# Kernel optimization log

Measured on AMD Instinct MI355X. Metric: run time of the kernel, lower is better.

Reference implementation:

```python
import jax, jax.numpy as jnp
import numpy as np

N_NODES = 20000
N_EDGES = 640000
C_IN = 128      # num_node_features
K_FOLDS = 8     # num_edge_features
FILTERS = 128


def setup_inputs() -> dict:
    key = jax.random.key(0)
    k1, k2, k3, k4, k5, k6 = jax.random.split(key, 6)
    node_features = jax.random.normal(k1, (N_NODES, C_IN), dtype=jnp.float32)
    edge_features = jax.random.uniform(k2, (K_FOLDS, N_EDGES), dtype=jnp.float32)
    rows = jax.random.randint(k3, (N_EDGES,), 0, N_NODES)
    cols = jax.random.randint(k4, (N_EDGES,), 0, N_NODES)
    indices = jnp.stack([rows, cols], axis=1).astype(jnp.int64)
    # glorot_uniform kernel [K, C_in, filters]
    limit = np.sqrt(6.0 / (C_IN + FILTERS))
    kernel = jax.random.uniform(k5, (K_FOLDS, C_IN, FILTERS), dtype=jnp.float32,
                                minval=-limit, maxval=limit)
    bias = jnp.zeros((FILTERS,), dtype=jnp.float32)
    return {
        "node_features": node_features,
        "edge_features": edge_features,
        "kernel": kernel,
        "bias": bias,
        "indices": indices,
        "out_size": N_NODES,
    }


def reference(node_features, edge_features, kernel, bias, indices, out_size):
    # fold_conv: out[i,f] = sum_{e: row(e)=i} sum_k ef[k,e] * (x[col(e)] @ kernel[k])[f]
    row = indices[:, 0]
    col = indices[:, 1]
    xg = node_features[col]  # [E, C] gathered source-node features
    E = xg.shape[0]
    msgs = jnp.zeros((E, kernel.shape[2]), dtype=node_features.dtype)
    # Loop over the small fixed number of folds (K=8); each iteration is a
    # dense [E,C]x[C,F] matmul scaled by the per-edge fold weight.
    for k in range(kernel.shape[0]):
        msgs = msgs + (xg @ kernel[k]) * edge_features[k][:, None]
    out = jax.ops.segment_sum(msgs, row, num_segments=out_size)  # [out_size, F]
    out = out + bias  # bias_add; activation is None (linear)
    return out
```

## Files before the change

### kernel.cpp

```cpp
#include <hip/hip_runtime.h>
#include <cstddef>
#include <cstdint>

static constexpr int kNodes   = 20000;
static constexpr int kEdges   = 640000;
static constexpr int kCin     = 128;
static constexpr int kFolds   = 8;
static constexpr int kFilters = 128;
static constexpr int kKdim    = kFolds * kCin;
static constexpr int kCap     = 80;

static constexpr int kNBucketF = 1250;
static constexpr int kCapF     = 768;
static constexpr int kBin1Blk  = 160;

typedef __attribute__((ext_vector_type(8))) short v8s;
typedef __attribute__((ext_vector_type(4))) float v4f;

__device__ __forceinline__ unsigned short f2bf(float f) {
    union { float f; uint32_t u; } v; v.f = f;
    const uint32_t u = v.u;
    return (unsigned short)((u + 0x7fffu + ((u >> 16) & 1u)) >> 16);
}
__device__ __forceinline__ float bf2f(unsigned short s) {
    union { uint32_t u; float f; } v; v.u = ((uint32_t)s) << 16;
    return v.f;
}

__global__ __launch_bounds__(256) void prep_k(
    const int2*  __restrict__ idx2,
    const float* __restrict__ ef,
    const float* __restrict__ x,
    const float* __restrict__ W,
    int* __restrict__ bucketCnt,
    unsigned int* __restrict__ pairs,
    unsigned int* __restrict__ rec,
    unsigned short* __restrict__ xb,
    unsigned short* __restrict__ Wp)
{
    const int b = blockIdx.x;
    const int t = threadIdx.x;
    if (b < kBin1Blk) {
        __shared__ int hist[kNBucketF];
        __shared__ int base[kNBucketF];
        const int e0 = b * 4096;

        for (int i = t; i < kNBucketF; i += 256) hist[i] = 0;
        __syncthreads();

        int rows[16];
        #pragma unroll
        for (int i = 0; i < 16; ++i) {
            const int e = e0 + i * 256 + t;
            int row = -1;
            if (e < kEdges) {
                row = idx2[e].x;
                atomicAdd(&hist[row >> 4], 1);
            }
            rows[i] = row;
        }
        __syncthreads();

        for (int i = t; i < kNBucketF; i += 256) {
            const int h = hist[i];
            base[i] = h ? atomicAdd(&bucketCnt[i], h) : 0;
            hist[i] = 0;
        }
        __syncthreads();

        #pragma unroll
        for (int i = 0; i < 16; ++i) {
            const int row = rows[i];
            if (row >= 0) {
                const int e  = e0 + i * 256 + t;
                const int bk = row >> 4;
                const int sl = base[bk] + atomicAdd(&hist[bk], 1);
                if (sl < kCapF)
                    pairs[(size_t)bk * kCapF + sl] =
                        ((unsigned)(row & 15) << 24) | (unsigned)e;
            }
        }
    } else if (b < 2660) {
        const int e = (b - kBin1Blk) * 256 + t;
        const int2 rc = idx2[e];
        union { uint4 q; unsigned int w[4]; unsigned short s[8]; } o;
        #pragma unroll
        for (int k = 0; k < kFolds; ++k)
            o.s[k] = f2bf(ef[(size_t)k * kEdges + e]);
        uint4* recp = (uint4*)(rec + (size_t)e * 8);
        recp[0] = make_uint4((unsigned)rc.y, o.w[0], o.w[1], o.w[2]);
        recp[1] = make_uint4(o.w[3], 0u, 0u, 0u);
    } else if (b < 3910) {
        const int i = (b - 2660) * 2048 + t * 8;
        const float4 a = *(const float4*)(x + i);
        const float4 c = *(const float4*)(x + i + 4);
        union { uint4 q; unsigned short s[8]; } o;
        o.s[0] = f2bf(a.x); o.s[1] = f2bf(a.y); o.s[2] = f2bf(a.z); o.s[3] = f2bf(a.w);
        o.s[4] = f2bf(c.x); o.s[5] = f2bf(c.y); o.s[6] = f2bf(c.z); o.s[7] = f2bf(c.w);
        *(uint4*)(xb + i) = o.q;
    } else {
        const int t2 = (b - 3910) * 256 + t;
        const int n  = t2 & 127;
        const int k8 = t2 >> 7;
        const int c  = k8 >> 2;
        const int q  = k8 & 3;
        union { uint4 qv; unsigned short s[8]; } o;
        #pragma unroll
        for (int j = 0; j < 8; ++j)
            o.s[j] = f2bf(W[(size_t)(k8 * 8 + j) * kFilters + n]);
        *(uint4*)(Wp + (((size_t)c * kFilters + n) * 4 + q) * 8) = o.qv;
    }
}

static constexpr int kSWS2 = 1048;

__global__ __launch_bounds__(256) void pull_k(
    const unsigned short* __restrict__ xb,
    const unsigned int* __restrict__ pairs,
    const int*  __restrict__ bucketCnt,
    const unsigned int* __restrict__ rec,
    const unsigned short* __restrict__ Wp,
    const float* __restrict__ bias,
    float* __restrict__ out)
{
    __shared__ int sCol[16][kCap + 4];
    __shared__ int sDeg[16];
    __shared__ int sCnt[16];
    __shared__ __align__(16) char arena[16 * (kCap + 4) * 8 * 4];

    float (*sEf)[kCap + 4][8] = (float(*)[kCap + 4][8])arena;
    unsigned short (*sS)[kSWS2] = (unsigned short(*)[kSWS2])arena;

    const int t  = threadIdx.x;
    const int B  = blockIdx.x;
    const int n0 = B * 16;

    if (t < 16) sCnt[t] = 0;
    __syncthreads();
    {
        int nseg = bucketCnt[B];
        nseg = nseg < kCapF ? nseg : kCapF;
        const unsigned int* seg = pairs + (size_t)B * kCapF;
        for (int s = t; s < nseg; s += 256) {
            const unsigned p = seg[s];
            const int rl = (int)(p >> 24);
            const int c  = atomicAdd(&sCnt[rl], 1);
            if (c < kCap) sCol[rl][c] = (int)(p & 0xFFFFFFu);
        }
    }
    __syncthreads();

    {
        const int g16 = t >> 4;
        const int s0  = t & 15;
        int dg = sCnt[g16];
        dg = dg < kCap ? dg : kCap;
        for (int s = s0; s < dg; s += 16) {
            const int e = sCol[g16][s];
            const uint4 q0    = *(const uint4*)(rec + (size_t)e * 8);
            const unsigned w3 = rec[(size_t)e * 8 + 4];
            sCol[g16][s] = (int)q0.x;
            sEf[g16][s][0] = bf2f((unsigned short)(q0.y));
            sEf[g16][s][1] = bf2f((unsigned short)(q0.y >> 16));
            sEf[g16][s][2] = bf2f((unsigned short)(q0.z));
            sEf[g16][s][3] = bf2f((unsigned short)(q0.z >> 16));
            sEf[g16][s][4] = bf2f((unsigned short)(q0.w));
            sEf[g16][s][5] = bf2f((unsigned short)(q0.w >> 16));
            sEf[g16][s][6] = bf2f((unsigned short)(w3));
            sEf[g16][s][7] = bf2f((unsigned short)(w3 >> 16));
        }
        const int dgP = (dg + 3) & ~3;
        for (int s = dg + s0; s < dgP; s += 16) {
            sCol[g16][s] = 0;
            #pragma unroll
            for (int k = 0; k < kFolds; ++k) sEf[g16][s][k] = 0.f;
        }
        if (s0 == 0) sDeg[g16] = dg;
    }
    __syncthreads();

    const int wave = t >> 6;
    const int lane = t & 63;
    const int g    = lane >> 4;
    const int c8   = (lane & 15) * 8;
    const int ln   = wave * 4 + g;
    const int degP = (sDeg[ln] + 3) & ~3;

    float acc[8][8];
    #pragma unroll
    for (int k = 0; k < 8; ++k)
        #pragma unroll
        for (int j = 0; j < 8; ++j) acc[k][j] = 0.f;

    const unsigned short* xbase = xb + c8;

    auto proc = [&](v8s xv, int i) {
        float xf[8];
        #pragma unroll
        for (int jj = 0; jj < 8; ++jj) xf[jj] = bf2f((unsigned short)xv[jj]);
        const float4 wa = *(const float4*)&sEf[ln][i][0];
        const float4 wc = *(const float4*)&sEf[ln][i][4];
        const float w[8] = {wa.x, wa.y, wa.z, wa.w, wc.x, wc.y, wc.z, wc.w};
        #pragma unroll
        for (int k = 0; k < 8; ++k)
            #pragma unroll
            for (int jj = 0; jj < 8; ++jj)
                acc[k][jj] += w[k] * xf[jj];
    };

    v8s x0 = (v8s)0, x1 = (v8s)0, x2 = (v8s)0, x3 = (v8s)0;
    if (degP > 0) {
        x0 = *(const v8s*)(xbase + (size_t)sCol[ln][0] * kCin);
        x1 = *(const v8s*)(xbase + (size_t)sCol[ln][1] * kCin);
        x2 = *(const v8s*)(xbase + (size_t)sCol[ln][2] * kCin);
        x3 = *(const v8s*)(xbase + (size_t)sCol[ln][3] * kCin);
    }

    for (int i = 0; i < degP; i += 4) {
        const int j = (i + 4 < degP) ? (i + 4) : i;
        const v8s y0 = *(const v8s*)(xbase + (size_t)sCol[ln][j]     * kCin);
        const v8s y1 = *(const v8s*)(xbase + (size_t)sCol[ln][j + 1] * kCin);
        const v8s y2 = *(const v8s*)(xbase + (size_t)sCol[ln][j + 2] * kCin);
        const v8s y3 = *(const v8s*)(xbase + (size_t)sCol[ln][j + 3] * kCin);

        proc(x0, i); proc(x1, i + 1); proc(x2, i + 2); proc(x3, i + 3);

        x0 = y0; x1 = y1; x2 = y2; x3 = y3;
    }

    __syncthreads();
    #pragma unroll
    for (int k = 0; k < 8; ++k) {
        union { uint4 q; unsigned short s[8]; } o;
        #pragma unroll
        for (int j = 0; j < 8; ++j) o.s[j] = f2bf(acc[k][j]);
        *(uint4*)&sS[ln][k * kCin + c8] = o.q;
    }
    __syncthreads();

    const int quad = lane >> 4;
    const int r16  = lane & 15;

    v4f acc2[2];
    acc2[0] = (v4f){0.f, 0.f, 0.f, 0.f};
    acc2[1] = (v4f){0.f, 0.f, 0.f, 0.f};

    const unsigned short* wb0 = Wp + (((size_t)(wave * 32 + r16)) * 4 + quad) * 8;
    const unsigned short* wb1 = wb0 + 16 * 4 * 8;

    #pragma unroll 4
    for (int c = 0; c < 32; ++c) {
        const v8s a  = *(const v8s*)&sS[r16][c * 32 + quad * 8];
        const v8s b0 = *(const v8s*)(wb0 + (size_t)c * kFilters * 32);
        const v8s b1 = *(const v8s*)(wb1 + (size_t)c * kFilters * 32);
        acc2[0] = __builtin_amdgcn_mfma_f32_16x16x32_bf16(a, b0, acc2[0], 0, 0, 0);
        acc2[1] = __builtin_amdgcn_mfma_f32_16x16x32_bf16(a, b1, acc2[1], 0, 0, 0);
    }

    #pragma unroll
    for (int i = 0; i < 2; ++i) {
        const int n  = (wave * 2 + i) * 16 + r16;
        const float bv = bias[n];
        #pragma unroll
        for (int r = 0; r < 4; ++r) {
            const int m = n0 + quad * 4 + r;
            out[(size_t)m * kFilters + n] = acc2[i][r] + bv;
        }
    }
}

extern "C" void kernel_launch(void* const* d_in, const int* in_sizes, int n_in,
                              void* d_out, int out_size, void* d_ws, size_t ws_size,
                              hipStream_t stream) {
    const float* x    = (const float*)d_in[0];
    const float* ef   = (const float*)d_in[1];
    const float* W    = (const float*)d_in[2];
    const float* bias = (const float*)d_in[3];
    const int2*  idx2 = (const int2*)d_in[4];
    float* out = (float*)d_out;

    char* ws = (char*)d_ws;
    unsigned int*   pairs  = (unsigned int*)(ws);
    int*            bucketCnt = (int*)(ws + 3840000);
    unsigned int*   rec    = (unsigned int*)(ws + 40960000);
    unsigned short* xb     = (unsigned short*)(ws + 67840000);
    unsigned short* Wp     = (unsigned short*)(ws + 72960000);

    hipMemsetAsync(bucketCnt, 0, kNBucketF * sizeof(int), stream);

    prep_k<<<3974, 256, 0, stream>>>(idx2, ef, x, W, bucketCnt,
                                     pairs, rec, xb, Wp);
    pull_k<<<kNodes / 16, 256, 0, stream>>>(xb, pairs, bucketCnt, rec,
                                            Wp, bias, out);
}
```

Baseline: 153.6 us.

## Halve nodes per pull block to double grid size and cut register use

Row buckets now hold 8 destination nodes instead of 16, so the pull kernel launches 2500 blocks instead of 1250. Each wave gathers 2 nodes, with 32 lanes per node each handling 4 channels, which halves the accumulator registers per thread. The aim is better occupancy and more even load across compute units. In exchange, half of the MFMA rows are zero-padded and wasted, gathers use narrower 8-byte loads, and the packed weight matrix is read from L2 by twice as many blocks.

```diff
diff --git a/kernel.cpp b/kernel.cpp
--- a/kernel.cpp
+++ b/kernel.cpp
@@ -10,11 +10,12 @@
 static constexpr int kKdim    = kFolds * kCin;
 static constexpr int kCap     = 80;
 
-static constexpr int kNBucketF = 1250;
-static constexpr int kCapF     = 768;
+static constexpr int kNBucketF = 2500;
+static constexpr int kCapF     = 384;
 static constexpr int kBin1Blk  = 160;
 
 typedef __attribute__((ext_vector_type(8))) short v8s;
+typedef __attribute__((ext_vector_type(4))) short v4s;
 typedef __attribute__((ext_vector_type(4))) float v4f;
 
 __device__ __forceinline__ unsigned short f2bf(float f) {
@@ -55,7 +56,7 @@
             int row = -1;
             if (e < kEdges) {
                 row = idx2[e].x;
-                atomicAdd(&hist[row >> 4], 1);
+                atomicAdd(&hist[row >> 3], 1);
             }
             rows[i] = row;
         }
@@ -73,11 +74,11 @@
             const int row = rows[i];
             if (row >= 0) {
                 const int e  = e0 + i * 256 + t;
-                const int bk = row >> 4;
+                const int bk = row >> 3;
                 const int sl = base[bk] + atomicAdd(&hist[bk], 1);
                 if (sl < kCapF)
                     pairs[(size_t)bk * kCapF + sl] =
-                        ((unsigned)(row & 15) << 24) | (unsigned)e;
+                        ((unsigned)(row & 7) << 24) | (unsigned)e;
             }
         }
     } else if (b < 2660) {
@@ -123,19 +124,19 @@
     const float* __restrict__ bias,
     float* __restrict__ out)
 {
-    __shared__ int sCol[16][kCap + 4];
-    __shared__ int sDeg[16];
-    __shared__ int sCnt[16];
-    __shared__ __align__(16) char arena[16 * (kCap + 4) * 8 * 4];
+    __shared__ int sCol[8][kCap + 4];
+    __shared__ int sDeg[8];
+    __shared__ int sCnt[8];
+    __shared__ __align__(16) char arena[8 * (kCap + 4) * 8 * 4];
 
     float (*sEf)[kCap + 4][8] = (float(*)[kCap + 4][8])arena;
     unsigned short (*sS)[kSWS2] = (unsigned short(*)[kSWS2])arena;
 
     const int t  = threadIdx.x;
     const int B  = blockIdx.x;
-    const int n0 = B * 16;
-
-    if (t < 16) sCnt[t] = 0;
+    const int n0 = B * 8;
+
+    if (t < 8) sCnt[t] = 0;
     __syncthreads();
     {
         int nseg = bucketCnt[B];
@@ -151,77 +152,78 @@
     __syncthreads();
 
     {
-        const int g16 = t >> 4;
-        const int s0  = t & 15;
-        int dg = sCnt[g16];
+        const int g8 = t >> 5;
+        const int s0 = t & 31;
+        int dg = sCnt[g8];
         dg = dg < kCap ? dg : kCap;
-        for (int s = s0; s < dg; s += 16) {
-            const int e = sCol[g16][s];
+        for (int s = s0; s < dg; s += 32) {
+            const int e = sCol[g8][s];
             const uint4 q0    = *(const uint4*)(rec + (size_t)e * 8);
             const unsigned w3 = rec[(size_t)e * 8 + 4];
-            sCol[g16][s] = (int)q0.x;
-            sEf[g16][s][0] = bf2f((unsigned short)(q0.y));
-            sEf[g16][s][1] = bf2f((unsigned short)(q0.y >> 16));
-            sEf[g16][s][2] = bf2f((unsigned short)(q0.z));
-            sEf[g16][s][3] = bf2f((unsigned short)(q0.z >> 16));
-            sEf[g16][s][4] = bf2f((unsigned short)(q0.w));
-            sEf[g16][s][5] = bf2f((unsigned short)(q0.w >> 16));
-            sEf[g16][s][6] = bf2f((unsigned short)(w3));
-            sEf[g16][s][7] = bf2f((unsigned short)(w3 >> 16));
+            sCol[g8][s] = (int)q0.x;
+            sEf[g8][s][0] = bf2f((unsigned short)(q0.y));
+            sEf[g8][s][1] = bf2f((unsigned short)(q0.y >> 16));
+            sEf[g8][s][2] = bf2f((unsigned short)(q0.z));
+            sEf[g8][s][3] = bf2f((unsigned short)(q0.z >> 16));
+            sEf[g8][s][4] = bf2f((unsigned short)(q0.w));
+            sEf[g8][s][5] = bf2f((unsigned short)(q0.w >> 16));
+            sEf[g8][s][6] = bf2f((unsigned short)(w3));
+            sEf[g8][s][7] = bf2f((unsigned short)(w3 >> 16));
         }
         const int dgP = (dg + 3) & ~3;
-        for (int s = dg + s0; s < dgP; s += 16) {
-            sCol[g16][s] = 0;
+        for (int s = dg + s0; s < dgP; s += 32) {
+            sCol[g8][s] = 0;
             #pragma unroll
-            for (int k = 0; k < kFolds; ++k) sEf[g16][s][k] = 0.f;
-        }
-        if (s0 == 0) sDeg[g16] = dg;
+            for (int k = 0; k < kFolds; ++k) sEf[g8][s][k] = 0.f;
+        }
+        if (s0 == 0) sDeg[g8] = dg;
     }
     __syncthreads();
 
     const int wave = t >> 6;
     const int lane = t & 63;
-    const int g    = lane >> 4;
-    const int c8   = (lane & 15) * 8;
-    const int ln   = wave * 4 + g;
+    const int g2   = lane >> 5;
+    const int chl  = lane & 31;
+    const int c4   = chl * 4;
+    const int ln   = wave * 2 + g2;
     const int degP = (sDeg[ln] + 3) & ~3;
 
-    float acc[8][8];
+    float acc[8][4];
     #pragma unroll
     for (int k = 0; k < 8; ++k)
         #pragma unroll
-        for (int j = 0; j < 8; ++j) acc[k][j] = 0.f;
-
-    const unsigned short* xbase = xb + c8;
-
-    auto proc = [&](v8s xv, int i) {
-        float xf[8];
-        #pragma unroll
-        for (int jj = 0; jj < 8; ++jj) xf[jj] = bf2f((unsigned short)xv[jj]);
+        for (int j = 0; j < 4; ++j) acc[k][j] = 0.f;
+
+    const unsigned short* xbase = xb + c4;
+
+    auto proc = [&](v4s xv, int i) {
+        float xf[4];
+        #pragma unroll
+        for (int jj = 0; jj < 4; ++jj) xf[jj] = bf2f((unsigned short)xv[jj]);
         const float4 wa = *(const float4*)&sEf[ln][i][0];
         const float4 wc = *(const float4*)&sEf[ln][i][4];
         const float w[8] = {wa.x, wa.y, wa.z, wa.w, wc.x, wc.y, wc.z, wc.w};
         #pragma unroll
         for (int k = 0; k < 8; ++k)
             #pragma unroll
-            for (int jj = 0; jj < 8; ++jj)
+            for (int jj = 0; jj < 4; ++jj)
                 acc[k][jj] += w[k] * xf[jj];
     };
 
-    v8s x0 = (v8s)0, x1 = (v8s)0, x2 = (v8s)0, x3 = (v8s)0;
+    v4s x0 = (v4s)0, x1 = (v4s)0, x2 = (v4s)0, x3 = (v4s)0;
     if (degP > 0) {
-        x0 = *(const v8s*)(xbase + (size_t)sCol[ln][0] * kCin);
-        x1 = *(const v8s*)(xbase + (size_t)sCol[ln][1] * kCin);
-        x2 = *(const v8s*)(xbase + (size_t)sCol[ln][2] * kCin);
-        x3 = *(const v8s*)(xbase + (size_t)sCol[ln][3] * kCin);
+        x0 = *(const v4s*)(xbase + (size_t)sCol[ln][0] * kCin);
+        x1 = *(const v4s*)(xbase + (size_t)sCol[ln][1] * kCin);
+        x2 = *(const v4s*)(xbase + (size_t)sCol[ln][2] * kCin);
+        x3 = *(const v4s*)(xbase + (size_t)sCol[ln][3] * kCin);
     }
 
     for (int i = 0; i < degP; i += 4) {
         const int j = (i + 4 < degP) ? (i + 4) : i;
-        const v8s y0 = *(const v8s*)(xbase + (size_t)sCol[ln][j]     * kCin);
-        const v8s y1 = *(const v8s*)(xbase + (size_t)sCol[ln][j + 1] * kCin);
-        const v8s y2 = *(const v8s*)(xbase + (size_t)sCol[ln][j + 2] * kCin);
-        const v8s y3 = *(const v8s*)(xbase + (size_t)sCol[ln][j + 3] * kCin);
+        const v4s y0 = *(const v4s*)(xbase + (size_t)sCol[ln][j]     * kCin);
+        const v4s y1 = *(const v4s*)(xbase + (size_t)sCol[ln][j + 1] * kCin);
+        const v4s y2 = *(const v4s*)(xbase + (size_t)sCol[ln][j + 2] * kCin);
+        const v4s y3 = *(const v4s*)(xbase + (size_t)sCol[ln][j + 3] * kCin);
 
         proc(x0, i); proc(x1, i + 1); proc(x2, i + 2); proc(x3, i + 3);
 
@@ -231,10 +233,10 @@
     __syncthreads();
     #pragma unroll
     for (int k = 0; k < 8; ++k) {
-        union { uint4 q; unsigned short s[8]; } o;
-        #pragma unroll
-        for (int j = 0; j < 8; ++j) o.s[j] = f2bf(acc[k][j]);
-        *(uint4*)&sS[ln][k * kCin + c8] = o.q;
+        union { uint2 q; unsigned short s[4]; } o;
+        #pragma unroll
+        for (int j = 0; j < 4; ++j) o.s[j] = f2bf(acc[k][j]);
+        *(uint2*)&sS[ln][k * kCin + c4] = o.q;
     }
     __syncthreads();
 
@@ -250,21 +252,24 @@
 
     #pragma unroll 4
     for (int c = 0; c < 32; ++c) {
-        const v8s a  = *(const v8s*)&sS[r16][c * 32 + quad * 8];
+        v8s a = (v8s)0;
+        if (r16 < 8) a = *(const v8s*)&sS[r16][c * 32 + quad * 8];
         const v8s b0 = *(const v8s*)(wb0 + (size_t)c * kFilters * 32);
         const v8s b1 = *(const v8s*)(wb1 + (size_t)c * kFilters * 32);
         acc2[0] = __builtin_amdgcn_mfma_f32_16x16x32_bf16(a, b0, acc2[0], 0, 0, 0);
         acc2[1] = __builtin_amdgcn_mfma_f32_16x16x32_bf16(a, b1, acc2[1], 0, 0, 0);
     }
 
-    #pragma unroll
-    for (int i = 0; i < 2; ++i) {
-        const int n  = (wave * 2 + i) * 16 + r16;
-        const float bv = bias[n];
-        #pragma unroll
-        for (int r = 0; r < 4; ++r) {
-            const int m = n0 + quad * 4 + r;
-            out[(size_t)m * kFilters + n] = acc2[i][r] + bv;
+    if (quad < 2) {
+        #pragma unroll
+        for (int i = 0; i < 2; ++i) {
+            const int n  = (wave * 2 + i) * 16 + r16;
+            const float bv = bias[n];
+            #pragma unroll
+            for (int r = 0; r < 4; ++r) {
+                const int m = quad * 4 + r;
+                out[(size_t)(n0 + m) * kFilters + n] = acc2[i][r] + bv;
+            }
         }
     }
 }
@@ -290,6 +295,6 @@
 
     prep_k<<<3974, 256, 0, stream>>>(idx2, ef, x, W, bucketCnt,
                                      pairs, rec, xb, Wp);
-    pull_k<<<kNodes / 16, 256, 0, stream>>>(xb, pairs, bucketCnt, rec,
-                                            Wp, bias, out);
-}
+    pull_k<<<kNBucketF, 256, 0, stream>>>(xb, pairs, bucketCnt, rec,
+                                          Wp, bias, out);
+}
```

After: 169.2 us. 1.1x slower.
